# Optimization experiments

Measured on AMD Instinct MI355X. Metric: run time of the kernel, lower is better.

## Reference

```python
import jax, jax.numpy as jnp
import numpy as np

N_EMBD = 512
NUM_HEADS = 8
HEAD_SIZE = 64


def setup_inputs() -> dict:
    key = jax.random.key(0)
    ks = jax.random.split(key, 6)
    B, T, C, H, D = 64, 256, N_EMBD, NUM_HEADS, HEAD_SIZE
    s = 0.02
    return {
        "x": jax.random.normal(ks[0], (B, T, C), dtype=jnp.float32),
        "wq": jax.random.normal(ks[1], (H, C, D), dtype=jnp.float32) * s,
        "wk": jax.random.normal(ks[2], (H, C, D), dtype=jnp.float32) * s,
        "wv": jax.random.normal(ks[3], (H, C, D), dtype=jnp.float32) * s,
        "bq": jnp.zeros((H, D), dtype=jnp.float32),
        "bk": jnp.zeros((H, D), dtype=jnp.float32),
        "bv": jnp.zeros((H, D), dtype=jnp.float32),
        "wo": jax.random.normal(ks[4], (H * D, C), dtype=jnp.float32) * s,
        "bo": jnp.zeros((C,), dtype=jnp.float32),
    }


def reference(x, wq, wk, wv, bq, bk, bv, wo, bo):
    B, T, C = x.shape
    H, _, D = wq.shape
    # per-head QKV projections (vectorized over heads)
    q = jnp.einsum('btc,hcd->bhtd', x, wq) + bq[None, :, None, :]
    k = jnp.einsum('btc,hcd->bhtd', x, wk) + bk[None, :, None, :]
    v = jnp.einsum('btc,hcd->bhtd', x, wv) + bv[None, :, None, :]
    scale = 1.0 / jnp.sqrt(jnp.asarray(D, dtype=x.dtype))
    scores = jnp.einsum('bhtd,bhsd->bhts', q, k) * scale  # [B,H,T,T]
    causal = jnp.tril(jnp.ones((T, T), dtype=bool))
    scores = jnp.where(causal[None, None], scores, -jnp.inf)
    weights = jax.nn.softmax(scores, axis=-1)  # dropout omitted (eval mode)
    out = jnp.einsum('bhts,bhsd->bhtd', weights, v)  # [B,H,T,D]
    combined = out.transpose(0, 2, 1, 3).reshape(B, T, H * D)
    return combined @ wo + bo
```

## Files before the change

### kernel.cpp

```cpp
#include <hip/hip_runtime.h>

typedef unsigned int   u32;
typedef unsigned short u16;
typedef __attribute__((ext_vector_type(8))) short short8;
typedef __attribute__((ext_vector_type(4))) float f32x4;


__device__ __forceinline__ u16 f2bf(float f) {
    u32 u = __float_as_uint(f);
    u += 0x7fffu + ((u >> 16) & 1u);
    return (u16)(u >> 16);
}

__device__ __forceinline__ void gload_lds16(const u16* g, u16* l) {
    __builtin_amdgcn_global_load_lds(
        (const __attribute__((address_space(1))) u32*)(const void*)g,
        (__attribute__((address_space(3))) u32*)(void*)l, 16, 0, 0);
}

__global__ void cast_x_kernel(const float* __restrict__ x, u16* __restrict__ xb) {
    int i = blockIdx.x * 256 + threadIdx.x;
    float4 v = ((const float4*)x)[i];
    ushort4 o;
    o.x = f2bf(v.x); o.y = f2bf(v.y); o.z = f2bf(v.z); o.w = f2bf(v.w);
    ((ushort4*)xb)[i] = o;
}

__global__ void pack_wqkv_kernel(const float* __restrict__ wq, const float* __restrict__ wk,
                                 const float* __restrict__ wv, u16* __restrict__ wt) {
    int i = blockIdx.x * 256 + threadIdx.x;
    int n = i >> 9, c = i & 511;
    int proj = n >> 9, hd = n & 511;
    int h = hd >> 6, d = hd & 63;
    const float* w = (proj == 0) ? wq : (proj == 1) ? wk : wv;
    wt[(size_t)n * 512 + c] = f2bf(w[h * 32768 + c * 64 + d]);
}

__global__ void pack_wo_kernel(const float* __restrict__ wo, u16* __restrict__ wt) {
    int i = blockIdx.x * 256 + threadIdx.x;
    int n = i >> 9, k = i & 511;
    wt[(size_t)n * 512 + k] = f2bf(wo[(size_t)k * 512 + n]);
}

template<int EPI, int NT>
__global__ __launch_bounds__(256)
void gemm128_kernel(const u16* __restrict__ A, const u16* __restrict__ Bt,
                    float* __restrict__ outf, const float* __restrict__ bo,
                    u16* __restrict__ Qb, u16* __restrict__ Kb, u16* __restrict__ Vb,
                    const float* __restrict__ bq, const float* __restrict__ bk,
                    const float* __restrict__ bv) {
    __shared__ __align__(16) u16 As[2][128 * 32];
    __shared__ __align__(16) u16 Bs[2][128 * 32];
    const int tid = threadIdx.x;
    const int bid = blockIdx.x;
    const int xcd = bid & 7;
    const int k8  = bid >> 3;
    const int m0 = (xcd * 16 + k8 / NT) * 128;
    const int n0 = (k8 % NT) * 128;
    const int lrow = tid >> 2;
    const int seg  = tid & 3;
    const int xsw  = (lrow >> 1) & 3;
    const u16* Ag = A  + (size_t)(m0 + lrow) * 512 + (seg ^ xsw) * 8;
    const u16* Bg = Bt + (size_t)(n0 + lrow) * 512 + (seg ^ xsw) * 8;
    const int lofs = lrow * 32 + seg * 8;

    const int w = tid >> 6, lane = tid & 63;
    const int wrow = (w >> 1) * 64, wcol = (w & 1) * 64;
    const int lm = lane & 15, quad = lane >> 4;
    const int kx = (quad ^ ((lm >> 1) & 3)) * 8;

    f32x4 acc[4][4] = {};

    gload_lds16(Ag,            As[0] + lofs);
    gload_lds16(Ag + 64 * 512, As[0] + lofs + 64 * 32);
    gload_lds16(Bg,            Bs[0] + lofs);
    gload_lds16(Bg + 64 * 512, Bs[0] + lofs + 64 * 32);

    #pragma unroll 2
    for (int kt = 0; kt < 16; ++kt) {
        __syncthreads();
        if (kt < 15) {
            const u16* Agp = Ag + (kt + 1) * 32;
            const u16* Bgp = Bg + (kt + 1) * 32;
            u16* Asp = As[(kt + 1) & 1] + lofs;
            u16* Bsp = Bs[(kt + 1) & 1] + lofs;
            gload_lds16(Agp,            Asp);
            gload_lds16(Agp + 64 * 512, Asp + 64 * 32);
            gload_lds16(Bgp,            Bsp);
            gload_lds16(Bgp + 64 * 512, Bsp + 64 * 32);
        }
        const u16* Ac = As[kt & 1];
        const u16* Bc = Bs[kt & 1];
        short8 af[4], bf[4];
        #pragma unroll
        for (int mi = 0; mi < 4; ++mi)
            af[mi] = *(const short8*)(Ac + (wrow + mi * 16 + lm) * 32 + kx);
        #pragma unroll
        for (int ni = 0; ni < 4; ++ni)
            bf[ni] = *(const short8*)(Bc + (wcol + ni * 16 + lm) * 32 + kx);
        #pragma unroll
        for (int mi = 0; mi < 4; ++mi)
            #pragma unroll
            for (int ni = 0; ni < 4; ++ni)
                acc[mi][ni] = __builtin_amdgcn_mfma_f32_16x16x32_bf16(af[mi], bf[ni], acc[mi][ni], 0, 0, 0);
    }

    if (EPI == 1) {
        #pragma unroll
        for (int ni = 0; ni < 4; ++ni) {
            int ncol = n0 + wcol + ni * 16 + lm;
            float bias = bo[ncol];
            #pragma unroll
            for (int mi = 0; mi < 4; ++mi) {
                int mbase = m0 + wrow + mi * 16 + quad * 4;
                #pragma unroll
                for (int r = 0; r < 4; ++r)
                    outf[(size_t)(mbase + r) * 512 + ncol] = acc[mi][ni][r] + bias;
            }
        }
    } else {
        #pragma unroll
        for (int ni = 0; ni < 4; ++ni) {
            int ncol = n0 + wcol + ni * 16 + lm;
            int proj = ncol >> 9, hd = ncol & 511;
            int h = hd >> 6, d = hd & 63;
            const float* bptr = (proj == 0) ? bq : (proj == 1) ? bk : bv;
            u16* dst = (proj == 0) ? Qb : (proj == 1) ? Kb : Vb;
            float bias = bptr[hd];
            #pragma unroll
            for (int mi = 0; mi < 4; ++mi) {
                int mbase = m0 + wrow + mi * 16 + quad * 4;
                #pragma unroll
                for (int r = 0; r < 4; ++r) {
                    int mrow = mbase + r;
                    int b = mrow >> 8, t = mrow & 255;
                    size_t idx = (proj == 2)
                        ? ((size_t)((b * 8 + h) * 64 + d) * 256 + t)
                        : ((size_t)((b * 8 + h) * 256 + t) * 64 + d);
                    dst[idx] = f2bf(acc[mi][ni][r] + bias);
                }
            }
        }
    }
}

__global__ __launch_bounds__(256)
void attn_mfma_kernel(const u16* __restrict__ Qg, const u16* __restrict__ Kg,
                      const u16* __restrict__ Vtg, u16* __restrict__ attn) {
    __shared__ __align__(16) u16 lds[20480];
    const int bid = blockIdx.x;
    const int head = (bid & 7) * 64 + ((bid >> 3) >> 1);
    const int iset = (bid >> 3) & 1;
    const int b = head >> 3, h = head & 7;
    const int tid = threadIdx.x;
    const size_t hb = (size_t)head * 16384;

    {
        const uint4* Ksrc = (const uint4*)(Kg + hb);
        uint4* L4 = (uint4*)lds;
        #pragma unroll
        for (int it = 0; it < 8; ++it) {
            int g = it * 256 + tid;
            int kr = g >> 3, kc = g & 7;
            L4[kr * 8 + (kc ^ (kr & 7))] = Ksrc[g];
        }
    }
    __syncthreads();

    const int w = tid >> 6, lane = tid & 63;
    const int lm = lane & 15, quad = lane >> 4;
    const int l7 = lm & 7;

    const int kx0 = (quad ^ l7) * 8;
    const int kx1 = ((4 + quad) ^ l7) * 8;
    const u16* Kbase = lds + lm * 64;
    const u16* Vg = Vtg + hb;
    const int Pbase = 16384 + w * 1024;
    const int x0 = (lm >> 3) & 1;
    const int pw_even = Pbase + quad * 16 + l7 + x0 * 8;
    const int pw_odd  = Pbase + quad * 16 + l7 + (x0 ^ 1) * 8;
    const int pr0 = Pbase + ((lm & 3) * 4 + (quad >> 1)) * 64
                  + (2 * (lm >> 2) + ((quad & 1) ^ (lm & 1))) * 8;

    #pragma unroll 1
    for (int ii = 0; ii < 2; ++ii) {
        const int i = iset ? (ii ? 2 : 1) : (ii ? 3 : 0);
        const int t0 = i * 64 + w * 16;
        short8 qa0 = *(const short8*)(Qg + hb + (size_t)(t0 + lm) * 64 + quad * 8);
        short8 qa1 = *(const short8*)(Qg + hb + (size_t)(t0 + lm) * 64 + 32 + quad * 8);
        f32x4 O[4] = {};
        float mr[4] = {-INFINITY, -INFINITY, -INFINITY, -INFINITY};
        float lr[4] = {0.f, 0.f, 0.f, 0.f};

        #pragma unroll 1
        for (int j = 0; j <= i; ++j) {
            f32x4 S[4] = {};
            #pragma unroll
            for (int ni = 0; ni < 4; ++ni) {
                const u16* kp = Kbase + j * 4096 + ni * 1024;
                short8 kb0 = *(const short8*)(kp + kx0);
                short8 kb1 = *(const short8*)(kp + kx1);
                S[ni] = __builtin_amdgcn_mfma_f32_16x16x32_bf16(qa0, kb0, S[ni], 0, 0, 0);
                S[ni] = __builtin_amdgcn_mfma_f32_16x16x32_bf16(qa1, kb1, S[ni], 0, 0, 0);
            }
            if (j == i) {
                #pragma unroll
                for (int ni = 0; ni < 4; ++ni) {
                    int scol = ni * 16 + lm;
                    #pragma unroll
                    for (int rr = 0; rr < 4; ++rr) {
                        int tloc = w * 16 + quad * 4 + rr;
                        S[ni][rr] = (scol > tloc) ? -INFINITY : S[ni][rr] * 0.125f;
                    }
                }
            } else {
                #pragma unroll
                for (int ni = 0; ni < 4; ++ni)
                    #pragma unroll
                    for (int rr = 0; rr < 4; ++rr)
                        S[ni][rr] *= 0.125f;
            }
            float alpha[4];
            #pragma unroll
            for (int rr = 0; rr < 4; ++rr) {
                float mx = fmaxf(fmaxf(S[0][rr], S[1][rr]), fmaxf(S[2][rr], S[3][rr]));
                mx = fmaxf(mx, __shfl_xor(mx, 1));
                mx = fmaxf(mx, __shfl_xor(mx, 2));
                mx = fmaxf(mx, __shfl_xor(mx, 4));
                mx = fmaxf(mx, __shfl_xor(mx, 8));
                float mnew = fmaxf(mr[rr], mx);
                alpha[rr] = __expf(mr[rr] - mnew);
                mr[rr] = mnew;
            }
            float rs[4] = {0.f, 0.f, 0.f, 0.f};
            #pragma unroll
            for (int ni = 0; ni < 4; ++ni) {
                #pragma unroll
                for (int rr = 0; rr < 4; ++rr) {
                    float p = __expf(S[ni][rr] - mr[rr]);
                    rs[rr] += p;
                    int addr = ((rr & 1) ? pw_odd : pw_even) + (rr * 4 + ni) * 64;
                    lds[addr] = f2bf(p);
                }
            }
            #pragma unroll
            for (int rr = 0; rr < 4; ++rr) {
                float s = rs[rr];
                s += __shfl_xor(s, 1);
                s += __shfl_xor(s, 2);
                s += __shfl_xor(s, 4);
                s += __shfl_xor(s, 8);
                lr[rr] = lr[rr] * alpha[rr] + s;
                O[0][rr] *= alpha[rr]; O[1][rr] *= alpha[rr];
                O[2][rr] *= alpha[rr]; O[3][rr] *= alpha[rr];
            }
            __syncthreads();
            short8 pa0 = *(const short8*)(lds + pr0);
            short8 pa1 = *(const short8*)(lds + pr0 + 128);
            #pragma unroll
            for (int nd = 0; nd < 4; ++nd) {
                const u16* vp = Vg + (size_t)(nd * 16 + lm) * 256 + j * 64;
                short8 vb0 = *(const short8*)(vp + quad * 8);
                short8 vb1 = *(const short8*)(vp + 32 + quad * 8);
                O[nd] = __builtin_amdgcn_mfma_f32_16x16x32_bf16(pa0, vb0, O[nd], 0, 0, 0);
                O[nd] = __builtin_amdgcn_mfma_f32_16x16x32_bf16(pa1, vb1, O[nd], 0, 0, 0);
            }
        }
        #pragma unroll
        for (int rr = 0; rr < 4; ++rr) {
            float inv = 1.0f / lr[rr];
            int t = t0 + quad * 4 + rr;
            u16* op = attn + (size_t)(b * 256 + t) * 512 + h * 64 + lm;
            op[0]  = f2bf(O[0][rr] * inv);
            op[16] = f2bf(O[1][rr] * inv);
            op[32] = f2bf(O[2][rr] * inv);
            op[48] = f2bf(O[3][rr] * inv);
        }
    }
}

extern "C" void kernel_launch(void* const* d_in, const int* in_sizes, int n_in,
                              void* d_out, int out_size, void* d_ws, size_t ws_size,
                              hipStream_t stream) {
    const float* x  = (const float*)d_in[0];
    const float* wq = (const float*)d_in[1];
    const float* wk = (const float*)d_in[2];
    const float* wv = (const float*)d_in[3];
    const float* bq = (const float*)d_in[4];
    const float* bk = (const float*)d_in[5];
    const float* bv = (const float*)d_in[6];
    const float* wo = (const float*)d_in[7];
    const float* bo = (const float*)d_in[8];
    float* out = (float*)d_out;

    char* ws = (char*)d_ws;
    const size_t SZ = 16777216;
    u16* xb    = (u16*)(ws);
    u16* Qb    = (u16*)(ws + SZ);
    u16* Kb    = (u16*)(ws + 2 * SZ);
    u16* Vt    = (u16*)(ws + 3 * SZ);
    u16* attn  = (u16*)(ws + 4 * SZ);
    u16* wqkvT = (u16*)(ws + 5 * SZ);
    u16* woT   = (u16*)(ws + 5 * SZ + 1572864);

    cast_x_kernel<<<8192, 256, 0, stream>>>(x, xb);
    pack_wqkv_kernel<<<3072, 256, 0, stream>>>(wq, wk, wv, wqkvT);
    pack_wo_kernel<<<1024, 256, 0, stream>>>(wo, woT);

    gemm128_kernel<0, 12><<<1536, 256, 0, stream>>>(
        xb, wqkvT, nullptr, nullptr, Qb, Kb, Vt, bq, bk, bv);

    attn_mfma_kernel<<<1024, 256, 0, stream>>>(Qb, Kb, Vt, attn);

    gemm128_kernel<1, 4><<<512, 256, 0, stream>>>(
        attn, woT, out, bo, nullptr, nullptr, nullptr, nullptr, nullptr, nullptr);
}
```

Measured before the change: 211.7 us.

## Retile QKV and output GEMMs and prefetch V fragments in attention

The QKV projection GEMM becomes a 256x128 tile with each wave owning 64x128 and 8 accumulator columns, which halves the block count and raises reuse of each loaded B tile. The output GEMM shrinks to a 128x64 tile so it launches more blocks and fills the device better. In the attention kernel, V fragments are loaded from global memory right after the QK MFMAs, before the softmax, so their latency can hide behind the softmax math. The trade-offs are more registers per thread in the QKV GEMM and more B-tile reloads in the output GEMM.

```diff
diff --git a/kernel.cpp b/kernel.cpp
--- a/kernel.cpp
+++ b/kernel.cpp
@@ -42,21 +42,19 @@
     wt[(size_t)n * 512 + k] = f2bf(wo[(size_t)k * 512 + n]);
 }
 
-template<int EPI, int NT>
-__global__ __launch_bounds__(256)
-void gemm128_kernel(const u16* __restrict__ A, const u16* __restrict__ Bt,
-                    float* __restrict__ outf, const float* __restrict__ bo,
-                    u16* __restrict__ Qb, u16* __restrict__ Kb, u16* __restrict__ Vb,
-                    const float* __restrict__ bq, const float* __restrict__ bk,
-                    const float* __restrict__ bv) {
-    __shared__ __align__(16) u16 As[2][128 * 32];
+__global__ __launch_bounds__(256, 2)
+void gemm_qkv(const u16* __restrict__ A, const u16* __restrict__ Bt,
+              u16* __restrict__ Qb, u16* __restrict__ Kb, u16* __restrict__ Vb,
+              const float* __restrict__ bq, const float* __restrict__ bk,
+              const float* __restrict__ bv) {
+    __shared__ __align__(16) u16 As[2][256 * 32];
     __shared__ __align__(16) u16 Bs[2][128 * 32];
     const int tid = threadIdx.x;
     const int bid = blockIdx.x;
     const int xcd = bid & 7;
     const int k8  = bid >> 3;
-    const int m0 = (xcd * 16 + k8 / NT) * 128;
-    const int n0 = (k8 % NT) * 128;
+    const int m0 = (xcd * 8 + k8 / 12) * 256;
+    const int n0 = (k8 % 12) * 128;
     const int lrow = tid >> 2;
     const int seg  = tid & 3;
     const int xsw  = (lrow >> 1) & 3;
@@ -65,16 +63,102 @@
     const int lofs = lrow * 32 + seg * 8;
 
     const int w = tid >> 6, lane = tid & 63;
-    const int wrow = (w >> 1) * 64, wcol = (w & 1) * 64;
+    const int wrow = w * 64;
     const int lm = lane & 15, quad = lane >> 4;
     const int kx = (quad ^ ((lm >> 1) & 3)) * 8;
 
-    f32x4 acc[4][4] = {};
+    f32x4 acc[4][8] = {};
+
+    #pragma unroll
+    for (int j = 0; j < 4; ++j)
+        gload_lds16(Ag + j * 64 * 512, As[0] + lofs + j * 2048);
+    #pragma unroll
+    for (int j = 0; j < 2; ++j)
+        gload_lds16(Bg + j * 64 * 512, Bs[0] + lofs + j * 2048);
+
+    #pragma unroll 2
+    for (int kt = 0; kt < 16; ++kt) {
+        __syncthreads();
+        if (kt < 15) {
+            const u16* Agp = Ag + (kt + 1) * 32;
+            const u16* Bgp = Bg + (kt + 1) * 32;
+            u16* Asp = As[(kt + 1) & 1] + lofs;
+            u16* Bsp = Bs[(kt + 1) & 1] + lofs;
+            #pragma unroll
+            for (int j = 0; j < 4; ++j)
+                gload_lds16(Agp + j * 64 * 512, Asp + j * 2048);
+            #pragma unroll
+            for (int j = 0; j < 2; ++j)
+                gload_lds16(Bgp + j * 64 * 512, Bsp + j * 2048);
+        }
+        const u16* Ac = As[kt & 1];
+        const u16* Bc = Bs[kt & 1];
+        short8 af[4], bf[8];
+        #pragma unroll
+        for (int mi = 0; mi < 4; ++mi)
+            af[mi] = *(const short8*)(Ac + (wrow + mi * 16 + lm) * 32 + kx);
+        #pragma unroll
+        for (int ni = 0; ni < 8; ++ni)
+            bf[ni] = *(const short8*)(Bc + (ni * 16 + lm) * 32 + kx);
+        #pragma unroll
+        for (int mi = 0; mi < 4; ++mi)
+            #pragma unroll
+            for (int ni = 0; ni < 8; ++ni)
+                acc[mi][ni] = __builtin_amdgcn_mfma_f32_16x16x32_bf16(af[mi], bf[ni], acc[mi][ni], 0, 0, 0);
+    }
+
+    #pragma unroll
+    for (int ni = 0; ni < 8; ++ni) {
+        int ncol = n0 + ni * 16 + lm;
+        int proj = ncol >> 9, hd = ncol & 511;
+        int h = hd >> 6, d = hd & 63;
+        const float* bptr = (proj == 0) ? bq : (proj == 1) ? bk : bv;
+        u16* dst = (proj == 0) ? Qb : (proj == 1) ? Kb : Vb;
+        float bias = bptr[hd];
+        #pragma unroll
+        for (int mi = 0; mi < 4; ++mi) {
+            int mbase = m0 + wrow + mi * 16 + quad * 4;
+            #pragma unroll
+            for (int r = 0; r < 4; ++r) {
+                int mrow = mbase + r;
+                int b = mrow >> 8, t = mrow & 255;
+                size_t idx = (proj == 2)
+                    ? ((size_t)((b * 8 + h) * 64 + d) * 256 + t)
+                    : ((size_t)((b * 8 + h) * 256 + t) * 64 + d);
+                dst[idx] = f2bf(acc[mi][ni][r] + bias);
+            }
+        }
+    }
+}
+
+__global__ __launch_bounds__(256)
+void gemm_out(const u16* __restrict__ A, const u16* __restrict__ Bt,
+              float* __restrict__ outf, const float* __restrict__ bo) {
+    __shared__ __align__(16) u16 As[2][128 * 32];
+    __shared__ __align__(16) u16 Bs[2][64 * 32];
+    const int tid = threadIdx.x;
+    const int bid = blockIdx.x;
+    const int xcd = bid & 7;
+    const int k8  = bid >> 3;
+    const int m0 = (xcd * 16 + k8 / 8) * 128;
+    const int n0 = (k8 % 8) * 64;
+    const int lrow = tid >> 2;
+    const int seg  = tid & 3;
+    const int xsw  = (lrow >> 1) & 3;
+    const u16* Ag = A  + (size_t)(m0 + lrow) * 512 + (seg ^ xsw) * 8;
+    const u16* Bg = Bt + (size_t)(n0 + lrow) * 512 + (seg ^ xsw) * 8;
+    const int lofs = lrow * 32 + seg * 8;
+
+    const int w = tid >> 6, lane = tid & 63;
+    const int wrow = w * 32;
+    const int lm = lane & 15, quad = lane >> 4;
+    const int kx = (quad ^ ((lm >> 1) & 3)) * 8;
+
+    f32x4 acc[2][4] = {};
 
     gload_lds16(Ag,            As[0] + lofs);
-    gload_lds16(Ag + 64 * 512, As[0] + lofs + 64 * 32);
+    gload_lds16(Ag + 64 * 512, As[0] + lofs + 2048);
     gload_lds16(Bg,            Bs[0] + lofs);
-    gload_lds16(Bg + 64 * 512, Bs[0] + lofs + 64 * 32);
 
     #pragma unroll 2
     for (int kt = 0; kt < 16; ++kt) {
@@ -85,61 +169,35 @@
             u16* Asp = As[(kt + 1) & 1] + lofs;
             u16* Bsp = Bs[(kt + 1) & 1] + lofs;
             gload_lds16(Agp,            Asp);
-            gload_lds16(Agp + 64 * 512, Asp + 64 * 32);
+            gload_lds16(Agp + 64 * 512, Asp + 2048);
             gload_lds16(Bgp,            Bsp);
-            gload_lds16(Bgp + 64 * 512, Bsp + 64 * 32);
         }
         const u16* Ac = As[kt & 1];
         const u16* Bc = Bs[kt & 1];
-        short8 af[4], bf[4];
-        #pragma unroll
-        for (int mi = 0; mi < 4; ++mi)
+        short8 af[2], bf[4];
+        #pragma unroll
+        for (int mi = 0; mi < 2; ++mi)
             af[mi] = *(const short8*)(Ac + (wrow + mi * 16 + lm) * 32 + kx);
         #pragma unroll
         for (int ni = 0; ni < 4; ++ni)
-            bf[ni] = *(const short8*)(Bc + (wcol + ni * 16 + lm) * 32 + kx);
-        #pragma unroll
-        for (int mi = 0; mi < 4; ++mi)
+            bf[ni] = *(const short8*)(Bc + (ni * 16 + lm) * 32 + kx);
+        #pragma unroll
+        for (int mi = 0; mi < 2; ++mi)
             #pragma unroll
             for (int ni = 0; ni < 4; ++ni)
                 acc[mi][ni] = __builtin_amdgcn_mfma_f32_16x16x32_bf16(af[mi], bf[ni], acc[mi][ni], 0, 0, 0);
     }
 
-    if (EPI == 1) {
-        #pragma unroll
-        for (int ni = 0; ni < 4; ++ni) {
-            int ncol = n0 + wcol + ni * 16 + lm;
-            float bias = bo[ncol];
-            #pragma unroll
-            for (int mi = 0; mi < 4; ++mi) {
-                int mbase = m0 + wrow + mi * 16 + quad * 4;
-                #pragma unroll
-                for (int r = 0; r < 4; ++r)
-                    outf[(size_t)(mbase + r) * 512 + ncol] = acc[mi][ni][r] + bias;
-            }
-        }
-    } else {
-        #pragma unroll
-        for (int ni = 0; ni < 4; ++ni) {
-            int ncol = n0 + wcol + ni * 16 + lm;
-            int proj = ncol >> 9, hd = ncol & 511;
-            int h = hd >> 6, d = hd & 63;
-            const float* bptr = (proj == 0) ? bq : (proj == 1) ? bk : bv;
-            u16* dst = (proj == 0) ? Qb : (proj == 1) ? Kb : Vb;
-            float bias = bptr[hd];
-            #pragma unroll
-            for (int mi = 0; mi < 4; ++mi) {
-                int mbase = m0 + wrow + mi * 16 + quad * 4;
-                #pragma unroll
-                for (int r = 0; r < 4; ++r) {
-                    int mrow = mbase + r;
-                    int b = mrow >> 8, t = mrow & 255;
-                    size_t idx = (proj == 2)
-                        ? ((size_t)((b * 8 + h) * 64 + d) * 256 + t)
-                        : ((size_t)((b * 8 + h) * 256 + t) * 64 + d);
-                    dst[idx] = f2bf(acc[mi][ni][r] + bias);
-                }
-            }
+    #pragma unroll
+    for (int ni = 0; ni < 4; ++ni) {
+        int ncol = n0 + ni * 16 + lm;
+        float bias = bo[ncol];
+        #pragma unroll
+        for (int mi = 0; mi < 2; ++mi) {
+            int mbase = m0 + wrow + mi * 16 + quad * 4;
+            #pragma unroll
+            for (int r = 0; r < 4; ++r)
+                outf[(size_t)(mbase + r) * 512 + ncol] = acc[mi][ni][r] + bias;
         }
     }
 }
@@ -202,6 +260,13 @@
                 short8 kb1 = *(const short8*)(kp + kx1);
                 S[ni] = __builtin_amdgcn_mfma_f32_16x16x32_bf16(qa0, kb0, S[ni], 0, 0, 0);
                 S[ni] = __builtin_amdgcn_mfma_f32_16x16x32_bf16(qa1, kb1, S[ni], 0, 0, 0);
+            }
+            short8 vb[4][2];
+            #pragma unroll
+            for (int nd = 0; nd < 4; ++nd) {
+                const u16* vp = Vg + (size_t)(nd * 16 + lm) * 256 + j * 64;
+                vb[nd][0] = *(const short8*)(vp + quad * 8);
+                vb[nd][1] = *(const short8*)(vp + 32 + quad * 8);
             }
             if (j == i) {
                 #pragma unroll
@@ -259,11 +324,8 @@
             short8 pa1 = *(const short8*)(lds + pr0 + 128);
             #pragma unroll
             for (int nd = 0; nd < 4; ++nd) {
-                const u16* vp = Vg + (size_t)(nd * 16 + lm) * 256 + j * 64;
-                short8 vb0 = *(const short8*)(vp + quad * 8);
-                short8 vb1 = *(const short8*)(vp + 32 + quad * 8);
-                O[nd] = __builtin_amdgcn_mfma_f32_16x16x32_bf16(pa0, vb0, O[nd], 0, 0, 0);
-                O[nd] = __builtin_amdgcn_mfma_f32_16x16x32_bf16(pa1, vb1, O[nd], 0, 0, 0);
+                O[nd] = __builtin_amdgcn_mfma_f32_16x16x32_bf16(pa0, vb[nd][0], O[nd], 0, 0, 0);
+                O[nd] = __builtin_amdgcn_mfma_f32_16x16x32_bf16(pa1, vb[nd][1], O[nd], 0, 0, 0);
             }
         }
         #pragma unroll
@@ -307,11 +369,9 @@
     pack_wqkv_kernel<<<3072, 256, 0, stream>>>(wq, wk, wv, wqkvT);
     pack_wo_kernel<<<1024, 256, 0, stream>>>(wo, woT);
 
-    gemm128_kernel<0, 12><<<1536, 256, 0, stream>>>(
-        xb, wqkvT, nullptr, nullptr, Qb, Kb, Vt, bq, bk, bv);
+    gemm_qkv<<<768, 256, 0, stream>>>(xb, wqkvT, Qb, Kb, Vt, bq, bk, bv);
 
     attn_mfma_kernel<<<1024, 256, 0, stream>>>(Qb, Kb, Vt, attn);
 
-    gemm128_kernel<1, 4><<<512, 256, 0, stream>>>(
-        attn, woT, out, bo, nullptr, nullptr, nullptr, nullptr, nullptr, nullptr);
-}
+    gemm_out<<<1024, 256, 0, stream>>>(attn, woT, out, bo);
+}
```

Result: slower. 218.8 us (+3.4%).
